# Optimization experiments

Measured on AMD Instinct MI355X. Metric: run time of the kernel, lower is better.

Reference implementation:

```python
import jax, jax.numpy as jnp
import numpy as np

WINDOW_SIZE = 128

def setup_inputs() -> dict:
    key = jax.random.key(0)
    kq, kk, kv = jax.random.split(key, 3)
    B, S, D = 4, 4096, 128
    q = jax.random.normal(kq, (B, S, D), dtype=jnp.float32)
    k = jax.random.normal(kk, (B, S, D), dtype=jnp.float32)
    v = jax.random.normal(kv, (B, S, D), dtype=jnp.float32)
    return {"q": q, "k": k, "v": v}

def reference(q, k, v):
    B, S, D = q.shape
    q = q / jnp.sqrt(jnp.asarray(D, q.dtype))
    # band mask: tril(window_size-1) & triu(-(window_size-1)) == |i - j| <= window_size-1
    i = jax.lax.broadcasted_iota(jnp.int32, (S, S), 0)
    j = jax.lax.broadcasted_iota(jnp.int32, (S, S), 1)
    mask = jnp.abs(i - j) <= (WINDOW_SIZE - 1)
    scores = jnp.einsum('bqd,bkd->bqk', q, k)  # [B,S,S]
    scores = jnp.where(mask, scores, jnp.asarray(-1e9, scores.dtype))
    weights = jax.nn.softmax(scores, axis=-1)
    return jnp.einsum('bqk,bkd->bqd', weights, v)
```

## Files before the change

### kernel.cpp

```cpp
#include <hip/hip_runtime.h>


typedef __attribute__((ext_vector_type(8))) _Float16 half8;
typedef __attribute__((ext_vector_type(2))) __fp16 fp16x2;
typedef __attribute__((ext_vector_type(4))) float floatx4;

#define MFMA_F16(a, b, c) __builtin_amdgcn_mfma_f32_16x16x32_f16(a, b, c, 0, 0, 0)

constexpr int S_ = 4096, D_ = 128, W_ = 127;
constexpr int BQ = 64, BK = 64;
constexpr int PST = 72;
constexpr int OST = 132;

union SMem {
  struct {
    _Float16 Kh[2][BK * D_];
    _Float16 Vt[2][D_ * BK];
    _Float16 Ps[4][16 * PST];
  } a;
  struct {
    float Om[8][16 * OST];
    float l_[8][16];
  } b;
};

__device__ __forceinline__ unsigned pk2(float a, float b) {
  union { fp16x2 h; unsigned u; } c;
  c.h = __builtin_amdgcn_cvt_pkrtz(a, b);
  return c.u;
}

__device__ __forceinline__ void gll16(const _Float16* g, _Float16* l) {
  __builtin_amdgcn_global_load_lds(
      (const __attribute__((address_space(1))) void*)g,
      (__attribute__((address_space(3))) void*)l, 16, 0, 0);
}

__global__ __launch_bounds__(256, 4)
void prep_kernel(const float* __restrict__ kg, const float* __restrict__ vg,
                 _Float16* __restrict__ K16, _Float16* __restrict__ Vt16)
{
  __shared__ __align__(16) _Float16 Vs[BK * D_];
  const int t  = threadIdx.x;
  const int bb = blockIdx.x >> 6;
  const int c  = blockIdx.x & 63;
  const size_t base = ((size_t)bb * S_ + c * 64) * D_;

#pragma unroll
  for (int j = 0; j < 4; ++j) {
    const int id = t + 256 * j;
    const int s = id >> 4, blk = id & 15;
    const float* src = kg + base + s * D_ + blk * 8;
    float4 a  = *(const float4*)src;
    float4 b2 = *(const float4*)(src + 4);
    uint4 w;
    w.x = pk2(a.x, a.y);  w.y = pk2(a.z, a.w);
    w.z = pk2(b2.x, b2.y); w.w = pk2(b2.z, b2.w);
    *(uint4*)(K16 + base + s * D_ + 8 * (blk ^ (s & 7))) = w;
  }

  const int vr = t >> 5, vc = t & 31;
  float4 vf[8];
#pragma unroll
  for (int u = 0; u < 8; ++u)
    vf[u] = *(const float4*)(vg + base + (8 * vr + u) * D_ + 4 * vc);
#pragma unroll
  for (int i = 0; i < 4; ++i) {
    uint4 tv;
    tv.x = pk2(((const float*)&vf[0])[i], ((const float*)&vf[1])[i]);
    tv.y = pk2(((const float*)&vf[2])[i], ((const float*)&vf[3])[i]);
    tv.z = pk2(((const float*)&vf[4])[i], ((const float*)&vf[5])[i]);
    tv.w = pk2(((const float*)&vf[6])[i], ((const float*)&vf[7])[i]);
    const int d = 4 * vc + i;
    *(uint4*)(&Vs[d * 64 + 8 * (vr ^ (d & 7))]) = tv;
  }
  __syncthreads();
  _Float16* vdst = Vt16 + (size_t)(bb * 64 + c) * (D_ * 64);
#pragma unroll
  for (int i = 0; i < 4; ++i) {
    const int id2 = t + 256 * i;
    *(uint4*)(vdst + id2 * 8) = *(const uint4*)(&Vs[id2 * 8]);
  }
}

__global__ __launch_bounds__(512, 2)
void swa_v8_kernel(const float* __restrict__ qg,
                   const _Float16* __restrict__ K16,
                   const _Float16* __restrict__ Vt16,
                   float* __restrict__ og)
{
  __shared__ __align__(16) SMem sm;
  const int tid  = threadIdx.x;
  const int lane = tid & 63;
  const int wave = tid >> 6;
  const int lx   = lane & 15;
  const int quad = lane >> 4;
  const int tile = wave & 3;
  const int par  = wave >> 2;

  const int bid = blockIdx.x;
  const int lid = (bid & 7) * 32 + (bid >> 3);
  const int bb  = lid >> 6;
  const int q0  = (lid & 63) * BQ;

  const float* qb = qg + (size_t)bb * S_ * D_;
  float*       ob = og + (size_t)bb * S_ * D_;

  const int qrow = q0 + 16 * tile + lx;
  half8 qh[4], ql[4];
#pragma unroll
  for (int ks = 0; ks < 4; ++ks) {
    const float* p = qb + (size_t)qrow * D_ + 32 * ks + 8 * quad;
#pragma unroll
    for (int j = 0; j < 8; ++j) {
      float f = p[j];
      _Float16 h = (_Float16)f;
      qh[ks][j] = h;
      ql[ks][j] = (_Float16)(f - (float)h);
    }
  }

  floatx4 o[8];
#pragma unroll
  for (int dt = 0; dt < 8; ++dt) o[dt] = (floatx4){0.f, 0.f, 0.f, 0.f};
  float lp[4] = {0.f, 0.f, 0.f, 0.f};

  const int kstart = (q0 > W_) ? (q0 - W_) : 0;
  int kend = q0 + BQ - 1 + W_;
  if (kend > S_ - 1) kend = S_ - 1;
  const int c0 = kstart >> 6, c1 = kend >> 6;

  const int ilo = q0 + 16 * tile, ihi = ilo + 15;
  const float C1 = 0.12751727f, C2 = -5.7707802f;

  const int wk = (wave < 4) ? wave : (wave - 4);

  {
    const int b0 = c0 & 1;
    const _Float16* kcb = K16 + ((size_t)bb * S_ + c0 * 64) * D_;
    const _Float16* vcb = Vt16 + (size_t)(bb * 64 + c0) * (D_ * 64);
#pragma unroll
    for (int i = 0; i < 4; ++i) {
      const int ofs = (wk * 4 + i) * 512;
      if (wave < 4) gll16(kcb + ofs + lane * 8, &sm.a.Kh[b0][ofs]);
      else          gll16(vcb + ofs + lane * 8, &sm.a.Vt[b0][ofs]);
    }
  }

  for (int c = c0; c <= c1; ++c) {
    const int buf = c & 1;
    asm volatile("s_waitcnt vmcnt(0)" ::: "memory");
    __builtin_amdgcn_s_barrier();
    asm volatile("" ::: "memory");

    if (c < c1) {
      const _Float16* kcb = K16 + ((size_t)bb * S_ + (c + 1) * 64) * D_;
      const _Float16* vcb = Vt16 + (size_t)(bb * 64 + (c + 1)) * (D_ * 64);
#pragma unroll
      for (int i = 0; i < 4; ++i) {
        const int ofs = (wk * 4 + i) * 512;
        if (wave < 4) gll16(kcb + ofs + lane * 8, &sm.a.Kh[buf ^ 1][ofs]);
        else          gll16(vcb + ofs + lane * 8, &sm.a.Vt[buf ^ 1][ofs]);
      }
    }

    const int kc = c * BK;
    const int klo = kc + 32 * par;
    if (klo + 31 < ilo - W_ || klo > ihi + W_) continue;

    floatx4 acc[2];
#pragma unroll
    for (int h = 0; h < 2; ++h) acc[h] = (floatx4){0.f, 0.f, 0.f, 0.f};
#pragma unroll
    for (int ks = 0; ks < 4; ++ks) {
#pragma unroll
      for (int h = 0; h < 2; ++h) {
        const int ct = 2 * par + h;
        const int row = 16 * ct + lx;
        half8 bfr = *(const half8*)(
            &sm.a.Kh[buf][row * D_ + 8 * ((4 * ks + quad) ^ (lx & 7))]);
        acc[h] = MFMA_F16(qh[ks], bfr, acc[h]);
        acc[h] = MFMA_F16(ql[ks], bfr, acc[h]);
      }
    }

    const int ibase = q0 + 16 * tile + 4 * quad;
#pragma unroll
    for (int r = 0; r < 4; ++r) {
      const int i = ibase + r;
      float psum = 0.f;
#pragma unroll
      for (int h = 0; h < 2; ++h) {
        const int ct = 2 * par + h;
        const int col = kc + 16 * ct + lx;
        const bool v = (unsigned)(col - i + W_) <= (unsigned)(2 * W_);
        const float e = __builtin_amdgcn_exp2f(__builtin_fmaf(acc[h][r], C1, C2));
        const float p = v ? e : 0.f;
        psum += p;
        sm.a.Ps[tile][(4 * quad + r) * PST + 16 * ct + lx] = (_Float16)p;
      }
      lp[r] += psum;
    }
    asm volatile("s_waitcnt lgkmcnt(0)" ::: "memory");
    half8 pa = *(const half8*)(&sm.a.Ps[tile][lx * PST + 32 * par + 8 * quad]);

#pragma unroll
    for (int dt = 0; dt < 8; ++dt) {
      const int d = 16 * dt + lx;
      half8 vf = *(const half8*)(
          &sm.a.Vt[buf][d * 64 + 8 * ((4 * par + quad) ^ (d & 7))]);
      o[dt] = MFMA_F16(pa, vf, o[dt]);
    }
  }

#pragma unroll
  for (int r = 0; r < 4; ++r) {
    float s = lp[r];
    s += __shfl_xor(s, 1);
    s += __shfl_xor(s, 2);
    s += __shfl_xor(s, 4);
    s += __shfl_xor(s, 8);
    lp[r] = s;
  }

  __syncthreads();
#pragma unroll
  for (int dt = 0; dt < 8; ++dt)
#pragma unroll
    for (int r = 0; r < 4; ++r)
      sm.b.Om[wave][(4 * quad + r) * OST + 16 * dt + lx] = o[dt][r];
  if (lx == 0) {
#pragma unroll
    for (int r = 0; r < 4; ++r) sm.b.l_[wave][4 * quad + r] = lp[r];
  }
  __syncthreads();

  const int row = tid >> 3, cd = tid & 7;
  const int tl = row >> 4, r16 = row & 15;
  const float inv = 1.f / (sm.b.l_[tl][r16] + sm.b.l_[tl + 4][r16]);
  const float* Oa = &sm.b.Om[tl][r16 * OST + 16 * cd];
  const float* Ob = &sm.b.Om[tl + 4][r16 * OST + 16 * cd];
  float* dst = ob + (size_t)(q0 + row) * D_ + 16 * cd;
#pragma unroll
  for (int t = 0; t < 4; ++t) {
    float4 xa = *(const float4*)(Oa + 4 * t);
    float4 xb = *(const float4*)(Ob + 4 * t);
    float4 r4;
    r4.x = (xa.x + xb.x) * inv;
    r4.y = (xa.y + xb.y) * inv;
    r4.z = (xa.z + xb.z) * inv;
    r4.w = (xa.w + xb.w) * inv;
    *(float4*)(dst + 4 * t) = r4;
  }
}

extern "C" void kernel_launch(void* const* d_in, const int* in_sizes, int n_in,
                              void* d_out, int out_size, void* d_ws, size_t ws_size,
                              hipStream_t stream) {
  const float* q = (const float*)d_in[0];
  const float* k = (const float*)d_in[1];
  const float* v = (const float*)d_in[2];
  float* out = (float*)d_out;

  const int B = in_sizes[0] / (S_ * D_);
  _Float16* K16  = (_Float16*)d_ws;
  _Float16* Vt16 = (_Float16*)d_ws + (size_t)B * S_ * D_;

  prep_kernel<<<dim3(B * (S_ / BK)), dim3(256), 0, stream>>>(k, v, K16, Vt16);
  swa_v8_kernel<<<dim3(B * (S_ / BQ)), dim3(512), 0, stream>>>(q, K16, Vt16, out);
}
```

Before: 87.84 us.

## Triple-buffer K/V chunks with two-ahead prefetch and partial vmcnt waits

Grows the LDS K and V staging from two buffers to three and prefetches two chunks ahead, waiting only on the older loads (vmcnt(4)) instead of draining every load each iteration. The aim is to hide more global-to-LDS latency behind the MFMA work. It also remaps prep kernel block indices with the same XCD-style swizzle as the main kernel. The extra LDS buffer raises shared memory per block, which may limit the two-blocks-per-CU occupancy.

Result: no change. 87.91 us (+0.1%).

```diff
diff --git a/kernel.cpp b/kernel.cpp
--- a/kernel.cpp
+++ b/kernel.cpp
@@ -14,8 +14,8 @@
 
 union SMem {
   struct {
-    _Float16 Kh[2][BK * D_];
-    _Float16 Vt[2][D_ * BK];
+    _Float16 Kh[3][BK * D_];
+    _Float16 Vt[3][D_ * BK];
     _Float16 Ps[4][16 * PST];
   } a;
   struct {
@@ -41,9 +41,11 @@
                  _Float16* __restrict__ K16, _Float16* __restrict__ Vt16)
 {
   __shared__ __align__(16) _Float16 Vs[BK * D_];
-  const int t  = threadIdx.x;
-  const int bb = blockIdx.x >> 6;
-  const int c  = blockIdx.x & 63;
+  const int t   = threadIdx.x;
+  const int bid = blockIdx.x;
+  const int lid = (bid & 7) * 32 + (bid >> 3);
+  const int bb  = lid >> 6;
+  const int c   = lid & 63;
   const size_t base = ((size_t)bb * S_ + c * 64) * D_;
 
 #pragma unroll
@@ -84,7 +86,7 @@
 }
 
 __global__ __launch_bounds__(512, 2)
-void swa_v8_kernel(const float* __restrict__ qg,
+void swa_v9_kernel(const float* __restrict__ qg,
                    const _Float16* __restrict__ K16,
                    const _Float16* __restrict__ Vt16,
                    float* __restrict__ og)
@@ -135,82 +137,81 @@
 
   const int wk = (wave < 4) ? wave : (wave - 4);
 
-  {
-    const int b0 = c0 & 1;
-    const _Float16* kcb = K16 + ((size_t)bb * S_ + c0 * 64) * D_;
-    const _Float16* vcb = Vt16 + (size_t)(bb * 64 + c0) * (D_ * 64);
+  auto issue_chunk = [&](int cc, int bi) {
+    const _Float16* kcb = K16 + ((size_t)bb * S_ + cc * 64) * D_;
+    const _Float16* vcb = Vt16 + (size_t)(bb * 64 + cc) * (D_ * 64);
 #pragma unroll
     for (int i = 0; i < 4; ++i) {
       const int ofs = (wk * 4 + i) * 512;
-      if (wave < 4) gll16(kcb + ofs + lane * 8, &sm.a.Kh[b0][ofs]);
-      else          gll16(vcb + ofs + lane * 8, &sm.a.Vt[b0][ofs]);
-    }
-  }
-
+      if (wave < 4) gll16(kcb + ofs + lane * 8, &sm.a.Kh[bi][ofs]);
+      else          gll16(vcb + ofs + lane * 8, &sm.a.Vt[bi][ofs]);
+    }
+  };
+
+  issue_chunk(c0, 0);
+  if (c0 + 1 <= c1) issue_chunk(c0 + 1, 1);
+
+  int b = 0;
   for (int c = c0; c <= c1; ++c) {
-    const int buf = c & 1;
-    asm volatile("s_waitcnt vmcnt(0)" ::: "memory");
+    if (c < c1) asm volatile("s_waitcnt vmcnt(4)" ::: "memory");
+    else        asm volatile("s_waitcnt vmcnt(0)" ::: "memory");
     __builtin_amdgcn_s_barrier();
     asm volatile("" ::: "memory");
 
-    if (c < c1) {
-      const _Float16* kcb = K16 + ((size_t)bb * S_ + (c + 1) * 64) * D_;
-      const _Float16* vcb = Vt16 + (size_t)(bb * 64 + (c + 1)) * (D_ * 64);
-#pragma unroll
-      for (int i = 0; i < 4; ++i) {
-        const int ofs = (wk * 4 + i) * 512;
-        if (wave < 4) gll16(kcb + ofs + lane * 8, &sm.a.Kh[buf ^ 1][ofs]);
-        else          gll16(vcb + ofs + lane * 8, &sm.a.Vt[buf ^ 1][ofs]);
-      }
+    if (c + 2 <= c1) {
+      int b2 = b + 2; if (b2 >= 3) b2 -= 3;
+      issue_chunk(c + 2, b2);
     }
 
     const int kc = c * BK;
     const int klo = kc + 32 * par;
-    if (klo + 31 < ilo - W_ || klo > ihi + W_) continue;
-
-    floatx4 acc[2];
-#pragma unroll
-    for (int h = 0; h < 2; ++h) acc[h] = (floatx4){0.f, 0.f, 0.f, 0.f};
-#pragma unroll
-    for (int ks = 0; ks < 4; ++ks) {
-#pragma unroll
-      for (int h = 0; h < 2; ++h) {
-        const int ct = 2 * par + h;
-        const int row = 16 * ct + lx;
-        half8 bfr = *(const half8*)(
-            &sm.a.Kh[buf][row * D_ + 8 * ((4 * ks + quad) ^ (lx & 7))]);
-        acc[h] = MFMA_F16(qh[ks], bfr, acc[h]);
-        acc[h] = MFMA_F16(ql[ks], bfr, acc[h]);
+    if (klo + 31 >= ilo - W_ && klo <= ihi + W_) {
+      floatx4 acc[2];
+#pragma unroll
+      for (int h = 0; h < 2; ++h) acc[h] = (floatx4){0.f, 0.f, 0.f, 0.f};
+#pragma unroll
+      for (int ks = 0; ks < 4; ++ks) {
+#pragma unroll
+        for (int h = 0; h < 2; ++h) {
+          const int ct = 2 * par + h;
+          const int row = 16 * ct + lx;
+          half8 bfr = *(const half8*)(
+              &sm.a.Kh[b][row * D_ + 8 * ((4 * ks + quad) ^ (lx & 7))]);
+          acc[h] = MFMA_F16(qh[ks], bfr, acc[h]);
+          acc[h] = MFMA_F16(ql[ks], bfr, acc[h]);
+        }
       }
-    }
-
-    const int ibase = q0 + 16 * tile + 4 * quad;
-#pragma unroll
-    for (int r = 0; r < 4; ++r) {
-      const int i = ibase + r;
-      float psum = 0.f;
-#pragma unroll
-      for (int h = 0; h < 2; ++h) {
-        const int ct = 2 * par + h;
-        const int col = kc + 16 * ct + lx;
-        const bool v = (unsigned)(col - i + W_) <= (unsigned)(2 * W_);
-        const float e = __builtin_amdgcn_exp2f(__builtin_fmaf(acc[h][r], C1, C2));
-        const float p = v ? e : 0.f;
-        psum += p;
-        sm.a.Ps[tile][(4 * quad + r) * PST + 16 * ct + lx] = (_Float16)p;
+
+      const int ibase = q0 + 16 * tile + 4 * quad;
+#pragma unroll
+      for (int r = 0; r < 4; ++r) {
+        const int i = ibase + r;
+        float psum = 0.f;
+#pragma unroll
+        for (int h = 0; h < 2; ++h) {
+          const int ct = 2 * par + h;
+          const int col = kc + 16 * ct + lx;
+          const bool v = (unsigned)(col - i + W_) <= (unsigned)(2 * W_);
+          const float e = __builtin_amdgcn_exp2f(__builtin_fmaf(acc[h][r], C1, C2));
+          const float p = v ? e : 0.f;
+          psum += p;
+          sm.a.Ps[tile][(4 * quad + r) * PST + 16 * ct + lx] = (_Float16)p;
+        }
+        lp[r] += psum;
       }
-      lp[r] += psum;
-    }
-    asm volatile("s_waitcnt lgkmcnt(0)" ::: "memory");
-    half8 pa = *(const half8*)(&sm.a.Ps[tile][lx * PST + 32 * par + 8 * quad]);
-
-#pragma unroll
-    for (int dt = 0; dt < 8; ++dt) {
-      const int d = 16 * dt + lx;
-      half8 vf = *(const half8*)(
-          &sm.a.Vt[buf][d * 64 + 8 * ((4 * par + quad) ^ (d & 7))]);
-      o[dt] = MFMA_F16(pa, vf, o[dt]);
-    }
+      asm volatile("s_waitcnt lgkmcnt(0)" ::: "memory");
+      half8 pa = *(const half8*)(&sm.a.Ps[tile][lx * PST + 32 * par + 8 * quad]);
+
+#pragma unroll
+      for (int dt = 0; dt < 8; ++dt) {
+        const int d = 16 * dt + lx;
+        half8 vf = *(const half8*)(
+            &sm.a.Vt[b][d * 64 + 8 * ((4 * par + quad) ^ (d & 7))]);
+        o[dt] = MFMA_F16(pa, vf, o[dt]);
+      }
+    }
+
+    b = (b == 2) ? 0 : b + 1;
   }
 
 #pragma unroll
@@ -267,5 +268,5 @@
   _Float16* Vt16 = (_Float16*)d_ws + (size_t)B * S_ * D_;
 
   prep_kernel<<<dim3(B * (S_ / BK)), dim3(256), 0, stream>>>(k, v, K16, Vt16);
-  swa_v8_kernel<<<dim3(B * (S_ / BQ)), dim3(512), 0, stream>>>(q, K16, Vt16, out);
-}
+  swa_v9_kernel<<<dim3(B * (S_ / BQ)), dim3(512), 0, stream>>>(q, K16, Vt16, out);
+}
```
